# Kernel optimization log

Hardware: AMD Instinct MI355X
Metric: run time of the kernel (lower is better)

Reference implementation:

```python
import jax, jax.numpy as jnp
import numpy as np

L = 16            # table_num (levels)
LOG2T = 14
T = 1 << LOG2T    # entries per table
Z = 512           # z_dim
S = 256           # style_dim
IMG = 256         # img_size
RES_MIN, RES_MAX = 16, 256
HID, OUT = 64, 3  # mlp hidden / out dims
B = 8
FDIM = 2 * L      # retrieved feature dim (2 per level)
PRIME = jnp.uint32(2654435761)  # instant-ngp hash prime
GAIN = 1.4142135623730951       # stylegan lrelu gain sqrt(2)
# geometric level resolutions res_min -> res_max
RES = np.floor(RES_MIN * np.exp(np.arange(L) * np.log(RES_MAX / RES_MIN) / (L - 1))).astype(np.float32)


def _lrelu(x):
    return GAIN * jnp.where(x >= 0, x, 0.2 * x)


def _coords():
    c = (jnp.arange(IMG, dtype=jnp.float32) + 0.5) / IMG
    x, y = jnp.meshgrid(c, c, indexing='ij')
    return jnp.stack((x, y), -1).reshape(-1, 2)  # (N, 2), N = IMG*IMG


def _mod_linear(x, s, aw, ab, w, b):
    # StyleGAN2-style modulated linear with demodulation. x: (B,N,in), s: (B,S)
    style = s @ aw + ab                                   # (B, in)
    demod = jax.lax.rsqrt((style ** 2) @ (w ** 2) + 1e-8)  # (B, out)
    return ((x * style[:, None, :]) @ w) * demod[:, None, :] + b


def _forward(z, mw0, mb0, mw1, mb1, mw2, mb2, base_tables, w_mod, b_mod,
             a0w, a0b, w0, bb0, a1w, a1b, w1, bb1, a2w, a2b, w2, bb2):
    s = _lrelu(z @ mw0 + mb0)
    s = _lrelu(s @ mw1 + mb1)
    s = _lrelu(s @ mw2 + mb2)                              # (B, S)
    # style-conditioned hash tables: per-level per-channel modulation of base tables
    scale = 1.0 + (s @ w_mod + b_mod).reshape(-1, L, 1, 2)
    tables = base_tables[None] * scale                     # (B, L, T, 2)

    coords = _coords()                                     # (N, 2)
    offs = jnp.array([[0, 0], [1, 0], [0, 1], [1, 1]], dtype=jnp.uint32)
    feats = []
    for l in range(L):
        pos = coords * RES[l]
        p0 = jnp.floor(pos)
        frac = pos - p0                                    # (N, 2)
        p0i = p0.astype(jnp.uint32)
        cx = p0i[None, :, 0] + offs[:, 0:1]                # (4, N)
        cy = p0i[None, :, 1] + offs[:, 1:2]
        idx = ((cx ^ (cy * PRIME)) & jnp.uint32(T - 1)).astype(jnp.int32)  # (4, N)
        wx = jnp.where(offs[:, 0:1] == 1, frac[None, :, 0], 1.0 - frac[None, :, 0])
        wy = jnp.where(offs[:, 1:2] == 1, frac[None, :, 1], 1.0 - frac[None, :, 1])
        wgt = wx * wy                                      # (4, N)
        tl = tables[:, l]                                  # (B, T, 2)
        f = jnp.take(tl, idx.reshape(-1), axis=1).reshape(tl.shape[0], 4, -1, 2)
        feats.append(jnp.einsum('bcnd,cn->bnd', f, wgt))   # bilinear interp
    h = jnp.concatenate(feats, -1)                         # (B, N, 2L)

    # stacked modulated MLP (3 layers), final tanh, then render to image
    h = _lrelu(_mod_linear(h, s, a0w, a0b, w0, bb0))
    h = _lrelu(_mod_linear(h, s, a1w, a1b, w1, bb1))
    h = jnp.tanh(_mod_linear(h, s, a2w, a2b, w2, bb2))     # (B, N, 3)
    return h.reshape(-1, IMG, IMG, OUT).transpose(0, 3, 1, 2)


def setup_inputs() -> dict:
    key = jax.random.key(0)
    ks = jax.random.split(key, 12)
    nrm = lambda k, sh, sc: jax.random.normal(k, sh, jnp.float32) * sc
    inp = {}
    inp['z'] = jax.random.normal(ks[0], (B, Z), jnp.float32)
    inp['mw0'] = nrm(ks[1], (Z, S), 1 / np.sqrt(Z)); inp['mb0'] = jnp.zeros((S,), jnp.float32)
    inp['mw1'] = nrm(ks[2], (S, S), 1 / np.sqrt(S)); inp['mb1'] = jnp.zeros((S,), jnp.float32)
    inp['mw2'] = nrm(ks[3], (S, S), 1 / np.sqrt(S)); inp['mb2'] = jnp.zeros((S,), jnp.float32)
    inp['base_tables'] = nrm(ks[4], (L, T, 2), 0.1)
    inp['w_mod'] = nrm(ks[5], (S, L * 2), 1 / np.sqrt(S)); inp['b_mod'] = jnp.zeros((L * 2,), jnp.float32)
    inp['a0w'] = nrm(ks[6], (S, FDIM), 1 / np.sqrt(S)); inp['a0b'] = jnp.ones((FDIM,), jnp.float32)
    inp['w0'] = nrm(ks[7], (FDIM, HID), 1 / np.sqrt(FDIM)); inp['bb0'] = jnp.zeros((HID,), jnp.float32)
    inp['a1w'] = nrm(ks[8], (S, HID), 1 / np.sqrt(S)); inp['a1b'] = jnp.ones((HID,), jnp.float32)
    inp['w1'] = nrm(ks[9], (HID, HID), 1 / np.sqrt(HID)); inp['bb1'] = jnp.zeros((HID,), jnp.float32)
    inp['a2w'] = nrm(ks[10], (S, HID), 1 / np.sqrt(S)); inp['a2b'] = jnp.ones((HID,), jnp.float32)
    inp['w2'] = nrm(ks[11], (HID, OUT), 1 / np.sqrt(HID)); inp['bb2'] = jnp.zeros((OUT,), jnp.float32)
    return inp


def reference(z, mw0, mb0, mw1, mb1, mw2, mb2, base_tables, w_mod, b_mod,
              a0w, a0b, w0, bb0, a1w, a1b, w1, bb1, a2w, a2b, w2, bb2):
    return _forward(z, mw0, mb0, mw1, mb1, mw2, mb2, base_tables, w_mod, b_mod,
                    a0w, a0b, w0, bb0, a1w, a1b, w1, bb1, a2w, a2b, w2, bb2)
```

## Files before the change

### kernel.cpp

```cpp
#include <hip/hip_runtime.h>
#include <hip/hip_bf16.h>

#define NLVL 16
#define TSZ  16384
#define NB   8

typedef _Float16 h8 __attribute__((ext_vector_type(8)));
typedef float    f4 __attribute__((ext_vector_type(4)));

#define MFMA16(A,B,C) __builtin_amdgcn_mfma_f32_16x16x32_f16(A,B,C,0,0,0)
#define GAINF 1.41421356237309515f

__device__ const float RES_TAB[16] = {
  16.f, 19.f, 23.f, 27.f, 33.f, 40.f, 48.f, 58.f,
  70.f, 84.f, 101.f, 122.f, 147.f, 176.f, 212.f, 255.f
};

__device__ __forceinline__ float lrelu(float x) {
  float v = x < 0.0f ? 0.2f * x : x;
  return GAINF * v;
}
__device__ __forceinline__ float act(float x) { return fmaxf(x, 0.2f * x); }

__device__ __forceinline__ float tanh_fast(float x) {
  float t = __builtin_amdgcn_exp2f(x * 2.8853900817779268f);
  return 1.0f - 2.0f * __builtin_amdgcn_rcpf(t + 1.0f);
}

__device__ __forceinline__ unsigned pk(float a, float b) {
  union { decltype(__builtin_amdgcn_cvt_pkrtz(0.f, 0.f)) h; unsigned u; } U;
  U.h = __builtin_amdgcn_cvt_pkrtz(a, b);
  return U.u;
}
__device__ __forceinline__ unsigned pk_rne(float a, float b) {
  union { _Float16 h[2]; unsigned u; } U;
  U.h[0] = (_Float16)a; U.h[1] = (_Float16)b;
  return U.u;
}

__device__ __forceinline__ void hash4(const float* __restrict__ bt,
                                      int n, int l0, float* g8)
{
  const float inv = 1.0f / 256.0f;
  float cx = ((n >> 8) + 0.5f) * inv;
  float cy = ((n & 255) + 0.5f) * inv;
#pragma unroll
  for (int j = 0; j < 4; ++j) {
    float res = RES_TAB[l0 + j];
    float px = cx * res, py = cy * res;
    float fx0 = floorf(px), fy0 = floorf(py);
    float fx = px - fx0, fy = py - fy0;
    unsigned x0 = (unsigned)fx0, y0 = (unsigned)fy0;
    unsigned hy0 = y0 * 2654435761u;
    unsigned hy1 = (y0 + 1u) * 2654435761u;
    unsigned i00 = (x0 ^ hy0) & 16383u;
    unsigned i10 = ((x0 + 1u) ^ hy0) & 16383u;
    unsigned i01 = (x0 ^ hy1) & 16383u;
    unsigned i11 = ((x0 + 1u) ^ hy1) & 16383u;
    const float2* tb = (const float2*)(bt + (size_t)(l0 + j) * (TSZ * 2));
    float2 f00 = tb[i00], f10 = tb[i10], f01 = tb[i01], f11 = tb[i11];
    float wx0 = 1.0f - fx, wy0 = 1.0f - fy;
    float w00 = wx0 * wy0, w10 = fx * wy0, w01 = wx0 * fy, w11 = fx * fy;
    g8[2 * j]     = w00 * f00.x + w10 * f10.x + w01 * f01.x + w11 * f11.x;
    g8[2 * j + 1] = w00 * f00.y + w10 * f10.y + w01 * f01.y + w11 * f11.y;
  }
}

__device__ __forceinline__ void hash_features(const float* __restrict__ bt,
                                              int n, float* g)
{
#pragma unroll
  for (int q = 0; q < 4; ++q) hash4(bt, n, q * 4, g + 8 * q);
}

__device__ __forceinline__ void map_layer(const float* __restrict__ xs_in,
                                          float* __restrict__ out_lds,
                                          const float* __restrict__ W,
                                          const float* __restrict__ bias,
                                          int K, int t,
                                          float* __restrict__ part)
{
  const int j4 = (t & 63) * 4;
  const int ks = t >> 6;
  const int chunk = K >> 2;
  const int kb = ks * chunk;
  f4 a0 = {0,0,0,0}, a1 = {0,0,0,0}, a2 = {0,0,0,0}, a3 = {0,0,0,0};
#pragma unroll 4
  for (int k = 0; k < chunk; k += 4) {
    f4 w0 = *(const f4*)&W[(kb + k + 0) * 256 + j4];
    f4 w1 = *(const f4*)&W[(kb + k + 1) * 256 + j4];
    f4 w2 = *(const f4*)&W[(kb + k + 2) * 256 + j4];
    f4 w3 = *(const f4*)&W[(kb + k + 3) * 256 + j4];
    float x0 = xs_in[kb + k + 0], x1 = xs_in[kb + k + 1];
    float x2 = xs_in[kb + k + 2], x3 = xs_in[kb + k + 3];
    a0 += x0 * w0; a1 += x1 * w1; a2 += x2 * w2; a3 += x3 * w3;
  }
  *(f4*)&part[ks * 256 + j4] = (a0 + a1) + (a2 + a3);
  __syncthreads();
  {
    float v = part[t] + part[256 + t] + part[512 + t] + part[768 + t];
    out_lds[t] = lrelu(bias[t] + v);
  }
  __syncthreads();
}

__global__ void __launch_bounds__(256) k_pre(
    const float* __restrict__ z,
    const float* __restrict__ mw0, const float* __restrict__ mb0,
    const float* __restrict__ mw1, const float* __restrict__ mb1,
    const float* __restrict__ mw2, const float* __restrict__ mb2,
    const float* __restrict__ bt,
    const float* __restrict__ w_mod, const float* __restrict__ b_mod,
    const float* __restrict__ a0w, const float* __restrict__ a0b,
    const float* __restrict__ w0,
    const float* __restrict__ a1w, const float* __restrict__ a1b,
    const float* __restrict__ w1,
    const float* __restrict__ a2w, const float* __restrict__ a2b,
    const float* __restrict__ w2,
    _Float16* __restrict__ W0h, _Float16* __restrict__ W1h,
    _Float16* __restrict__ W2h, _Float16* __restrict__ ghf)
{
  __shared__ __align__(16) unsigned smem[16384];

  const int t = threadIdx.x;

  if (blockIdx.x >= 8) {
    const int hb  = blockIdx.x - 8;
    const int lvl = hb & 15;
    const int pg  = hb >> 4;
    const int gg  = lvl >> 2;
    const int sub = 2 * (lvl & 3);

    const float4* tb4 = (const float4*)(bt + (size_t)lvl * (TSZ * 2));
#pragma unroll 8
    for (int i = 0; i < 32; ++i) {
      float4 v = tb4[i * 256 + t];
      int e = (i * 256 + t) * 2;
      smem[e]     = pk_rne(v.x, v.y);
      smem[e + 1] = pk_rne(v.z, v.w);
    }
    __syncthreads();

    const float res = RES_TAB[lvl];
    const float inv = 1.0f / 256.0f;
    float cy = (t + 0.5f) * inv;
    float py = cy * res;
    float fy0 = floorf(py);
    float fy = py - fy0;
    unsigned y0 = (unsigned)fy0;
    unsigned hy0 = y0 * 2654435761u;
    unsigned hy1 = (y0 + 1u) * 2654435761u;
    float wy0 = 1.0f - fy;

    const int xbase = pg * 32;
    const int cc = t & 15, th = t >> 4;
#pragma unroll 4
    for (int i = 0; i < 32; ++i) {
      float cx = (xbase + i + 0.5f) * inv;
      float px = cx * res;
      float fx0 = floorf(px);
      float fx = px - fx0;
      unsigned x0 = (unsigned)fx0;
      unsigned i00 = (x0 ^ hy0) & 16383u;
      unsigned i10 = ((x0 + 1u) ^ hy0) & 16383u;
      unsigned i01 = (x0 ^ hy1) & 16383u;
      unsigned i11 = ((x0 + 1u) ^ hy1) & 16383u;
      union { unsigned u; _Float16 h[2]; } e00, e10, e01, e11;
      e00.u = smem[i00]; e10.u = smem[i10];
      e01.u = smem[i01]; e11.u = smem[i11];
      float wx0 = 1.0f - fx;
      float w00 = wx0 * wy0, w10 = fx * wy0, w01 = wx0 * fy, w11 = fx * fy;
      float gx = w00 * (float)e00.h[0] + w10 * (float)e10.h[0]
               + w01 * (float)e01.h[0] + w11 * (float)e11.h[0];
      float gy = w00 * (float)e00.h[1] + w10 * (float)e10.h[1]
               + w01 * (float)e01.h[1] + w11 * (float)e11.h[1];
      int tile = pg * 512 + i * 16 + th;
      *(unsigned*)&ghf[(size_t)tile * 512 + (gg * 16 + cc) * 8 + sub] =
          pk_rne(gx, gy);
    }
    return;
  }

  float* xs   = (float*)smem;
  float* sA   = (float*)smem + 512;
  float* sB   = (float*)smem + 768;
  float* part = (float*)smem + 1024;
  float* st0  = (float*)smem + 3072;
  float* scf  = (float*)smem + 3104;
  float* st1  = (float*)smem + 3136;
  float* st2  = (float*)smem + 3200;
  float* dm0  = (float*)smem + 3264;
  float* dm1  = (float*)smem + 3328;
  float* dm2  = (float*)smem + 3392;

  const int b = blockIdx.x;

  for (int k = t; k < 512; k += 256) xs[k] = z[b * 512 + k];
  __syncthreads();

  map_layer(xs, sA, mw0, mb0, 512, t, part);
  map_layer(sA, sB, mw1, mb1, 256, t, part);
  map_layer(sB, xs, mw2, mb2, 256, t, part);
  const float* ss = xs;

  {
    const int jg = (t & 7) * 4, kc = t >> 3, kb = kc * 8;
    f4 am = {0,0,0,0}, as = {0,0,0,0};
#pragma unroll
    for (int k = 0; k < 8; ++k) {
      float sv = ss[kb + k];
      am += sv * *(const f4*)&w_mod[(kb + k) * 32 + jg];
      as += sv * *(const f4*)&a0w[(kb + k) * 32 + jg];
    }
    *(f4*)&part[kc * 32 + jg] = am;
    *(f4*)&part[1024 + kc * 32 + jg] = as;
  }
  __syncthreads();
  if (t < 32) {
    float am = b_mod[t], as = a0b[t];
#pragma unroll
    for (int q = 0; q < 32; ++q) { am += part[q * 32 + t]; as += part[1024 + q * 32 + t]; }
    scf[t] = 1.0f + am; st0[t] = as;
  }
  __syncthreads();
  {
    const int jg = (t & 15) * 4, kc = t >> 4, kb = kc * 16;
    f4 v1 = {0,0,0,0}, v2 = {0,0,0,0};
#pragma unroll
    for (int k = 0; k < 16; ++k) {
      float sv = ss[kb + k];
      v1 += sv * *(const f4*)&a1w[(kb + k) * 64 + jg];
      v2 += sv * *(const f4*)&a2w[(kb + k) * 64 + jg];
    }
    *(f4*)&part[kc * 64 + jg] = v1;
    *(f4*)&part[1024 + kc * 64 + jg] = v2;
  }
  __syncthreads();
  if (t >= 128 && t < 192) {
    int j = t - 128;
    float v1 = a1b[j], v2 = a2b[j];
#pragma unroll
    for (int q = 0; q < 16; ++q) { v1 += part[q * 64 + j]; v2 += part[1024 + q * 64 + j]; }
    st1[j] = v1; st2[j] = v2;
  }
  __syncthreads();

  if (t < 64) {
    float acc = 1e-8f;
    for (int i = 0; i < 32; ++i) { float p = st0[i] * w0[i * 64 + t]; acc = fmaf(p, p, acc); }
    dm0[t] = 1.0f / sqrtf(acc);
  }
  if (t >= 64 && t < 128) {
    int j = t - 64; float acc = 1e-8f;
    for (int k = 0; k < 64; ++k) { float p = st1[k] * w1[k * 64 + j]; acc = fmaf(p, p, acc); }
    dm1[j] = 1.0f / sqrtf(acc);
  }
  if (t >= 192 && t < 195) {
    int ch = t - 192; float acc = 1e-8f;
    for (int k = 0; k < 64; ++k) { float p = st2[k] * w2[k * 3 + ch]; acc = fmaf(p, p, acc); }
    dm2[ch] = 1.0f / sqrtf(acc);
  }
  __syncthreads();

  for (int f = t; f < 2048; f += 256) {
    int j = f >> 5, i = f & 31;
    W0h[b * 2048 + f] = (_Float16)(scf[i] * st0[i] * w0[i * 64 + j] * dm0[j]);
  }
  for (int f = t; f < 4096; f += 256) {
    int j2 = f >> 6, k = f & 63;
    W1h[b * 4096 + f] = (_Float16)(GAINF * st1[k] * w1[k * 64 + j2] * dm1[j2]);
  }
  for (int f = t; f < 1024; f += 256) {
    int ch = f >> 6, k = f & 63;
    W2h[b * 1024 + f] = (ch < 3) ? (_Float16)(GAINF * st2[k] * w2[k * 3 + ch] * dm2[ch])
                                 : (_Float16)0.0f;
  }
}

__device__ __forceinline__ void st4(_Float16* L, int pix, int jb, f4 v) {
  int ks = jb ^ ((pix & 7) << 3);
  union { unsigned u[2]; uint2 v2; } U;
  U.u[0] = pk(v[0], v[1]); U.u[1] = pk(v[2], v[3]);
  *(uint2*)(L + pix * 64 + ks) = U.v2;
}
__device__ __forceinline__ h8 ldf(const _Float16* L, int pix, int kb) {
  int ks = kb ^ ((pix & 7) << 3);
  return *(const h8*)(L + pix * 64 + ks);
}

template <int FUSED>
__global__ void __launch_bounds__(256) k_mlp(
    const _Float16* __restrict__ W0h, const _Float16* __restrict__ W1h,
    const _Float16* __restrict__ W2h, const _Float16* __restrict__ ghf,
    const float* __restrict__ bt,
    const float* __restrict__ bb0, const float* __restrict__ bb1,
    const float* __restrict__ bb2, float* __restrict__ out)
{
  __shared__ _Float16 lds[4][4096];
  __shared__ _Float16 hb[FUSED ? 8192 : 8];

  const int t = threadIdx.x;
  const int w = t >> 6, lane = t & 63;
  const int c = lane & 15, g = lane >> 4;
  const int b = blockIdx.y;
  const int pixb = blockIdx.x * 256 + w * 64;
  const int tile0 = pixb >> 4;
  _Float16* L = lds[w];

  if constexpr (FUSED) {
    float gl[32];
    hash_features(bt, blockIdx.x * 256 + t, gl);
    int tl = t >> 4, cl = t & 15;
#pragma unroll
    for (int gg = 0; gg < 4; ++gg) {
      union { unsigned u[4]; uint4 v; } U;
      U.u[0] = pk(gl[8 * gg + 0], gl[8 * gg + 1]);
      U.u[1] = pk(gl[8 * gg + 2], gl[8 * gg + 3]);
      U.u[2] = pk(gl[8 * gg + 4], gl[8 * gg + 5]);
      U.u[3] = pk(gl[8 * gg + 6], gl[8 * gg + 7]);
      *(uint4*)&hb[tl * 512 + (gg * 16 + cl) * 8] = U.v;
    }
    __syncthreads();
  }

  h8 A0[4], A1[4][2], A2[2];
#pragma unroll
  for (int jt = 0; jt < 4; ++jt)
    A0[jt] = *(const h8*)&W0h[b * 2048 + (jt * 16 + c) * 32 + 8 * g];
#pragma unroll
  for (int jt = 0; jt < 4; ++jt)
#pragma unroll
    for (int kf = 0; kf < 2; ++kf)
      A1[jt][kf] = *(const h8*)&W1h[b * 4096 + (jt * 16 + c) * 64 + kf * 32 + 8 * g];
#pragma unroll
  for (int kf = 0; kf < 2; ++kf)
    A2[kf] = *(const h8*)&W2h[b * 1024 + c * 64 + kf * 32 + 8 * g];

  f4 bv0[4], bv1[4], bv2;
#pragma unroll
  for (int jt = 0; jt < 4; ++jt) {
    bv0[jt] = *(const f4*)&bb0[jt * 16 + 4 * g];
    bv1[jt] = *(const f4*)&bb1[jt * 16 + 4 * g];
  }
  if (g == 0) { bv2 = f4{bb2[0], bb2[1], bb2[2], 0.0f}; }
  else        { bv2 = f4{0.0f, 0.0f, 0.0f, 0.0f}; }

  f4 acc[4][4];
#pragma unroll
  for (int pt = 0; pt < 4; ++pt) {
    h8 Bh;
    if constexpr (FUSED) {
      Bh = *(const h8*)&hb[(w * 4 + pt) * 512 + lane * 8];
    } else {
      Bh = *(const h8*)&ghf[(size_t)(tile0 + pt) * 512 + lane * 8];
    }
#pragma unroll
    for (int jt = 0; jt < 4; ++jt)
      acc[jt][pt] = MFMA16(A0[jt], Bh, bv0[jt]);
  }

#pragma unroll
  for (int jt = 0; jt < 4; ++jt)
#pragma unroll
    for (int pt = 0; pt < 4; ++pt) {
      f4 v = acc[jt][pt];
#pragma unroll
      for (int r = 0; r < 4; ++r) v[r] = act(v[r]);
      st4(L, pt * 16 + c, jt * 16 + 4 * g, v);
    }

  f4 acc1[4][4];
#pragma unroll
  for (int pt = 0; pt < 4; ++pt) {
    h8 Bf0 = ldf(L, pt * 16 + c, 0 * 32 + 8 * g);
    h8 Bf1 = ldf(L, pt * 16 + c, 1 * 32 + 8 * g);
#pragma unroll
    for (int jt = 0; jt < 4; ++jt) {
      f4 a = MFMA16(A1[jt][0], Bf0, bv1[jt]);
      acc1[jt][pt] = MFMA16(A1[jt][1], Bf1, a);
    }
  }

#pragma unroll
  for (int jt = 0; jt < 4; ++jt)
#pragma unroll
    for (int pt = 0; pt < 4; ++pt) {
      f4 v = acc1[jt][pt];
#pragma unroll
      for (int r = 0; r < 4; ++r) v[r] = act(v[r]);
      st4(L, pt * 16 + c, jt * 16 + 4 * g, v);
    }

#pragma unroll
  for (int pt = 0; pt < 4; ++pt) {
    h8 Bf0 = ldf(L, pt * 16 + c, 0 * 32 + 8 * g);
    h8 Bf1 = ldf(L, pt * 16 + c, 1 * 32 + 8 * g);
    f4 a = MFMA16(A2[0], Bf0, bv2);
    a = MFMA16(A2[1], Bf1, a);
    if (g == 0) {
      int pix = pixb + pt * 16 + c;
#pragma unroll
      for (int r = 0; r < 3; ++r)
        out[((b * 3 + r) << 16) + pix] = tanh_fast(a[r]);
    }
  }
}

extern "C" void kernel_launch(void* const* d_in, const int* in_sizes, int n_in,
                              void* d_out, int out_size, void* d_ws, size_t ws_size,
                              hipStream_t stream)
{
  const float* z    = (const float*)d_in[0];
  const float* mw0  = (const float*)d_in[1];
  const float* mb0  = (const float*)d_in[2];
  const float* mw1  = (const float*)d_in[3];
  const float* mb1  = (const float*)d_in[4];
  const float* mw2  = (const float*)d_in[5];
  const float* mb2  = (const float*)d_in[6];
  const float* bt   = (const float*)d_in[7];
  const float* wmod = (const float*)d_in[8];
  const float* bmod = (const float*)d_in[9];
  const float* a0w  = (const float*)d_in[10];
  const float* a0b  = (const float*)d_in[11];
  const float* w0   = (const float*)d_in[12];
  const float* bb0  = (const float*)d_in[13];
  const float* a1w  = (const float*)d_in[14];
  const float* a1b  = (const float*)d_in[15];
  const float* w1   = (const float*)d_in[16];
  const float* bb1  = (const float*)d_in[17];
  const float* a2w  = (const float*)d_in[18];
  const float* a2b  = (const float*)d_in[19];
  const float* w2   = (const float*)d_in[20];
  const float* bb2  = (const float*)d_in[21];

  char* ws = (char*)d_ws;
  _Float16* W0h = (_Float16*)(ws);
  _Float16* W1h = (_Float16*)(ws + 32768);
  _Float16* W2h = (_Float16*)(ws + 98304);
  _Float16* ghf = (_Float16*)(ws + 114688);
  float* out = (float*)d_out;

  if (ws_size >= (size_t)4308992) {
    k_pre<<<8 + 128, 256, 0, stream>>>(z, mw0, mb0, mw1, mb1, mw2, mb2, bt,
                                       wmod, bmod, a0w, a0b, w0,
                                       a1w, a1b, w1, a2w, a2b, w2,
                                       W0h, W1h, W2h, ghf);
    k_mlp<0><<<dim3(256, NB), 256, 0, stream>>>(W0h, W1h, W2h, ghf, bt,
                                                bb0, bb1, bb2, out);
  } else {
    k_pre<<<8, 256, 0, stream>>>(z, mw0, mb0, mw1, mb1, mw2, mb2, bt,
                                 wmod, bmod, a0w, a0b, w0,
                                 a1w, a1b, w1, a2w, a2b, w2,
                                 W0h, W1h, W2h, ghf);
    k_mlp<1><<<dim3(256, NB), 256, 0, stream>>>(W0h, W1h, W2h, ghf, bt,
                                                bb0, bb1, bb2, out);
  }
}
```

Measured before the change: 45.22 us.

## Run preprocessing kernel with 1024 threads, splitting reductions across more threads

The k_pre kernel moves from 256 to 1024 threads per block. The mapping-network layers, the style projections and the demodulation norms now split their K dimension over more threads, with larger partial-sum reductions held in LDS. The hash-grid blocks give each thread 8 x-columns instead of 32. This is meant to shorten the serial critical path of the small per-batch style computation and of the hash blocks, at the cost of longer LDS reduction loops and fewer resident blocks per CU.

```diff
diff --git a/kernel.cpp b/kernel.cpp
--- a/kernel.cpp
+++ b/kernel.cpp
@@ -65,7 +65,6 @@
     g8[2 * j + 1] = w00 * f00.y + w10 * f10.y + w01 * f01.y + w11 * f11.y;
   }
 }
-
 __device__ __forceinline__ void hash_features(const float* __restrict__ bt,
                                               int n, float* g)
 {
@@ -82,10 +81,10 @@
 {
   const int j4 = (t & 63) * 4;
   const int ks = t >> 6;
-  const int chunk = K >> 2;
+  const int chunk = K >> 4;
   const int kb = ks * chunk;
   f4 a0 = {0,0,0,0}, a1 = {0,0,0,0}, a2 = {0,0,0,0}, a3 = {0,0,0,0};
-#pragma unroll 4
+#pragma unroll 2
   for (int k = 0; k < chunk; k += 4) {
     f4 w0 = *(const f4*)&W[(kb + k + 0) * 256 + j4];
     f4 w1 = *(const f4*)&W[(kb + k + 1) * 256 + j4];
@@ -97,14 +96,16 @@
   }
   *(f4*)&part[ks * 256 + j4] = (a0 + a1) + (a2 + a3);
   __syncthreads();
-  {
-    float v = part[t] + part[256 + t] + part[512 + t] + part[768 + t];
+  if (t < 256) {
+    float v = 0.f;
+#pragma unroll
+    for (int q = 0; q < 16; ++q) v += part[q * 256 + t];
     out_lds[t] = lrelu(bias[t] + v);
   }
   __syncthreads();
 }
 
-__global__ void __launch_bounds__(256) k_pre(
+__global__ void __launch_bounds__(1024) k_pre(
     const float* __restrict__ z,
     const float* __restrict__ mw0, const float* __restrict__ mb0,
     const float* __restrict__ mw1, const float* __restrict__ mb1,
@@ -132,18 +133,19 @@
     const int sub = 2 * (lvl & 3);
 
     const float4* tb4 = (const float4*)(bt + (size_t)lvl * (TSZ * 2));
-#pragma unroll 8
-    for (int i = 0; i < 32; ++i) {
-      float4 v = tb4[i * 256 + t];
-      int e = (i * 256 + t) * 2;
+#pragma unroll
+    for (int i = 0; i < 8; ++i) {
+      float4 v = tb4[i * 1024 + t];
+      int e = (i * 1024 + t) * 2;
       smem[e]     = pk_rne(v.x, v.y);
       smem[e + 1] = pk_rne(v.z, v.w);
     }
     __syncthreads();
 
+    const int y = t & 255, xsub = t >> 8;
     const float res = RES_TAB[lvl];
     const float inv = 1.0f / 256.0f;
-    float cy = (t + 0.5f) * inv;
+    float cy = (y + 0.5f) * inv;
     float py = cy * res;
     float fy0 = floorf(py);
     float fy = py - fy0;
@@ -151,12 +153,12 @@
     unsigned hy0 = y0 * 2654435761u;
     unsigned hy1 = (y0 + 1u) * 2654435761u;
     float wy0 = 1.0f - fy;
-
-    const int xbase = pg * 32;
-    const int cc = t & 15, th = t >> 4;
-#pragma unroll 4
-    for (int i = 0; i < 32; ++i) {
-      float cx = (xbase + i + 0.5f) * inv;
+    const int cc = y & 15, th = y >> 4;
+
+#pragma unroll
+    for (int i = 0; i < 8; ++i) {
+      int xo = xsub * 8 + i;
+      float cx = (pg * 32 + xo + 0.5f) * inv;
       float px = cx * res;
       float fx0 = floorf(px);
       float fx = px - fx0;
@@ -174,28 +176,29 @@
                + w01 * (float)e01.h[0] + w11 * (float)e11.h[0];
       float gy = w00 * (float)e00.h[1] + w10 * (float)e10.h[1]
                + w01 * (float)e01.h[1] + w11 * (float)e11.h[1];
-      int tile = pg * 512 + i * 16 + th;
+      int tile = pg * 512 + xo * 16 + th;
       *(unsigned*)&ghf[(size_t)tile * 512 + (gg * 16 + cc) * 8 + sub] =
           pk_rne(gx, gy);
     }
     return;
   }
 
-  float* xs   = (float*)smem;
-  float* sA   = (float*)smem + 512;
-  float* sB   = (float*)smem + 768;
-  float* part = (float*)smem + 1024;
-  float* st0  = (float*)smem + 3072;
-  float* scf  = (float*)smem + 3104;
-  float* st1  = (float*)smem + 3136;
-  float* st2  = (float*)smem + 3200;
-  float* dm0  = (float*)smem + 3264;
-  float* dm1  = (float*)smem + 3328;
-  float* dm2  = (float*)smem + 3392;
+  float* F    = (float*)smem;
+  float* xs   = F;
+  float* sA   = F + 512;
+  float* sB   = F + 768;
+  float* st0  = F + 1024;
+  float* scf  = F + 1056;
+  float* st1  = F + 1088;
+  float* st2  = F + 1152;
+  float* dm0  = F + 1216;
+  float* dm1  = F + 1280;
+  float* dm2  = F + 1344;
+  float* part = F + 2048;
 
   const int b = blockIdx.x;
 
-  for (int k = t; k < 512; k += 256) xs[k] = z[b * 512 + k];
+  if (t < 512) xs[t] = z[b * 512 + t];
   __syncthreads();
 
   map_layer(xs, sA, mw0, mb0, 512, t, part);
@@ -204,74 +207,102 @@
   const float* ss = xs;
 
   {
-    const int jg = (t & 7) * 4, kc = t >> 3, kb = kc * 8;
+    const int jg = (t & 7) * 4, kc = t >> 3, kb = kc * 2;
     f4 am = {0,0,0,0}, as = {0,0,0,0};
 #pragma unroll
-    for (int k = 0; k < 8; ++k) {
+    for (int k = 0; k < 2; ++k) {
       float sv = ss[kb + k];
       am += sv * *(const f4*)&w_mod[(kb + k) * 32 + jg];
       as += sv * *(const f4*)&a0w[(kb + k) * 32 + jg];
     }
     *(f4*)&part[kc * 32 + jg] = am;
-    *(f4*)&part[1024 + kc * 32 + jg] = as;
+    *(f4*)&part[4096 + kc * 32 + jg] = as;
   }
   __syncthreads();
   if (t < 32) {
     float am = b_mod[t], as = a0b[t];
 #pragma unroll
-    for (int q = 0; q < 32; ++q) { am += part[q * 32 + t]; as += part[1024 + q * 32 + t]; }
+    for (int q = 0; q < 128; ++q) { am += part[q * 32 + t]; as += part[4096 + q * 32 + t]; }
     scf[t] = 1.0f + am; st0[t] = as;
   }
   __syncthreads();
+
   {
-    const int jg = (t & 15) * 4, kc = t >> 4, kb = kc * 16;
+    const int jg = (t & 15) * 4, kc = t >> 4, kb = kc * 4;
     f4 v1 = {0,0,0,0}, v2 = {0,0,0,0};
 #pragma unroll
-    for (int k = 0; k < 16; ++k) {
+    for (int k = 0; k < 4; ++k) {
       float sv = ss[kb + k];
       v1 += sv * *(const f4*)&a1w[(kb + k) * 64 + jg];
       v2 += sv * *(const f4*)&a2w[(kb + k) * 64 + jg];
     }
     *(f4*)&part[kc * 64 + jg] = v1;
-    *(f4*)&part[1024 + kc * 64 + jg] = v2;
+    *(f4*)&part[4096 + kc * 64 + jg] = v2;
   }
   __syncthreads();
   if (t >= 128 && t < 192) {
     int j = t - 128;
     float v1 = a1b[j], v2 = a2b[j];
 #pragma unroll
-    for (int q = 0; q < 16; ++q) { v1 += part[q * 64 + j]; v2 += part[1024 + q * 64 + j]; }
+    for (int q = 0; q < 64; ++q) { v1 += part[q * 64 + j]; v2 += part[4096 + q * 64 + j]; }
     st1[j] = v1; st2[j] = v2;
   }
   __syncthreads();
 
+  if (t < 256) {
+    int j = t & 63, q = t >> 6;
+    float acc = (q == 0) ? 1e-8f : 0.f;
+#pragma unroll
+    for (int i = q * 8; i < q * 8 + 8; ++i) {
+      float p = st0[i] * w0[i * 64 + j]; acc = fmaf(p, p, acc);
+    }
+    part[t] = acc;
+  } else if (t < 768) {
+    int u = t - 256, j = u & 63, q = u >> 6;
+    float acc = (q == 0) ? 1e-8f : 0.f;
+#pragma unroll
+    for (int k = q * 8; k < q * 8 + 8; ++k) {
+      float p = st1[k] * w1[k * 64 + j]; acc = fmaf(p, p, acc);
+    }
+    part[512 + u] = acc;
+  } else if (t < 832) {
+    int u = t - 768, ch = u & 3, q = u >> 2;
+    if (ch < 3) {
+      float acc = (q == 0) ? 1e-8f : 0.f;
+#pragma unroll
+      for (int k = q * 4; k < q * 4 + 4; ++k) {
+        float p = st2[k] * w2[k * 3 + ch]; acc = fmaf(p, p, acc);
+      }
+      part[1024 + u] = acc;
+    }
+  }
+  __syncthreads();
   if (t < 64) {
-    float acc = 1e-8f;
-    for (int i = 0; i < 32; ++i) { float p = st0[i] * w0[i * 64 + t]; acc = fmaf(p, p, acc); }
-    dm0[t] = 1.0f / sqrtf(acc);
-  }
-  if (t >= 64 && t < 128) {
-    int j = t - 64; float acc = 1e-8f;
-    for (int k = 0; k < 64; ++k) { float p = st1[k] * w1[k * 64 + j]; acc = fmaf(p, p, acc); }
-    dm1[j] = 1.0f / sqrtf(acc);
-  }
-  if (t >= 192 && t < 195) {
-    int ch = t - 192; float acc = 1e-8f;
-    for (int k = 0; k < 64; ++k) { float p = st2[k] * w2[k * 3 + ch]; acc = fmaf(p, p, acc); }
-    dm2[ch] = 1.0f / sqrtf(acc);
-  }
-  __syncthreads();
-
-  for (int f = t; f < 2048; f += 256) {
+    float a = part[t] + part[64 + t] + part[128 + t] + part[192 + t];
+    dm0[t] = 1.0f / sqrtf(a);
+  } else if (t < 128) {
+    int j = t - 64; float a = 0.f;
+#pragma unroll
+    for (int q = 0; q < 8; ++q) a += part[512 + q * 64 + j];
+    dm1[j] = 1.0f / sqrtf(a);
+  } else if (t >= 192 && t < 195) {
+    int ch = t - 192; float a = 0.f;
+#pragma unroll
+    for (int q = 0; q < 16; ++q) a += part[1024 + q * 4 + ch];
+    dm2[ch] = 1.0f / sqrtf(a);
+  }
+  __syncthreads();
+
+  for (int f = t; f < 2048; f += 1024) {
     int j = f >> 5, i = f & 31;
     W0h[b * 2048 + f] = (_Float16)(scf[i] * st0[i] * w0[i * 64 + j] * dm0[j]);
   }
-  for (int f = t; f < 4096; f += 256) {
+  for (int f = t; f < 4096; f += 1024) {
     int j2 = f >> 6, k = f & 63;
     W1h[b * 4096 + f] = (_Float16)(GAINF * st1[k] * w1[k * 64 + j2] * dm1[j2]);
   }
-  for (int f = t; f < 1024; f += 256) {
-    int ch = f >> 6, k = f & 63;
+  if (t < 1024) {
+    int f = t, ch = f >> 6, k = f & 63;
     W2h[b * 1024 + f] = (ch < 3) ? (_Float16)(GAINF * st2[k] * w2[k * 3 + ch] * dm2[ch])
                                  : (_Float16)0.0f;
   }
@@ -441,17 +472,17 @@
   float* out = (float*)d_out;
 
   if (ws_size >= (size_t)4308992) {
-    k_pre<<<8 + 128, 256, 0, stream>>>(z, mw0, mb0, mw1, mb1, mw2, mb2, bt,
-                                       wmod, bmod, a0w, a0b, w0,
-                                       a1w, a1b, w1, a2w, a2b, w2,
-                                       W0h, W1h, W2h, ghf);
+    k_pre<<<8 + 128, 1024, 0, stream>>>(z, mw0, mb0, mw1, mb1, mw2, mb2, bt,
+                                        wmod, bmod, a0w, a0b, w0,
+                                        a1w, a1b, w1, a2w, a2b, w2,
+                                        W0h, W1h, W2h, ghf);
     k_mlp<0><<<dim3(256, NB), 256, 0, stream>>>(W0h, W1h, W2h, ghf, bt,
                                                 bb0, bb1, bb2, out);
   } else {
-    k_pre<<<8, 256, 0, stream>>>(z, mw0, mb0, mw1, mb1, mw2, mb2, bt,
-                                 wmod, bmod, a0w, a0b, w0,
-                                 a1w, a1b, w1, a2w, a2b, w2,
-                                 W0h, W1h, W2h, ghf);
+    k_pre<<<8, 1024, 0, stream>>>(z, mw0, mb0, mw1, mb1, mw2, mb2, bt,
+                                  wmod, bmod, a0w, a0b, w0,
+                                  a1w, a1b, w1, a2w, a2b, w2,
+                                  W0h, W1h, W2h, ghf);
     k_mlp<1><<<dim3(256, NB), 256, 0, stream>>>(W0h, W1h, W2h, ghf, bt,
                                                 bb0, bb1, bb2, out);
   }
```

After: 45.06 us. No clear change (-0.3%).
